# Optimization experiments

Measured on AMD Instinct MI355X. Metric: run time of the kernel, lower is better.

Reference implementation:

```python
import jax, jax.numpy as jnp
import numpy as np

H = 2048  # hidden_dim == input_dim


def _lstm_step(x, h, c, Wih, Whh, bih, bhh):
    # x: [1, in], h/c: [1, H]; PyTorch gate order: i, f, g, o along 4H axis
    gates = x @ Wih.T + h @ Whh.T + bih + bhh  # [1, 4H]
    i, f, g, o = jnp.split(gates, 4, axis=-1)
    c2 = jax.nn.sigmoid(f) * c + jax.nn.sigmoid(i) * jnp.tanh(g)
    h2 = jax.nn.sigmoid(o) * jnp.tanh(c2)
    return h2, c2


def setup_inputs() -> dict:
    key = jax.random.key(0)
    ks = jax.random.split(key, 20)
    s = 0.02
    inp = {
        "x": jax.random.normal(ks[0], (1,), dtype=jnp.float32),
        "input_hidden": jax.random.normal(ks[1], (3, 1, H), dtype=jnp.float32),
        "input_cell": jax.random.normal(ks[2], (3, 1, H), dtype=jnp.float32),
        # layer 0: input_size = 1
        "Wih0": jax.random.normal(ks[3], (4 * H, 1), dtype=jnp.float32) * s,
        "Whh0": jax.random.normal(ks[4], (4 * H, H), dtype=jnp.float32) * s,
        "bih0": jax.random.normal(ks[5], (4 * H,), dtype=jnp.float32) * s,
        "bhh0": jax.random.normal(ks[6], (4 * H,), dtype=jnp.float32) * s,
        # layers 1, 2: input_size = H
        "Wih1": jax.random.normal(ks[7], (4 * H, H), dtype=jnp.float32) * s,
        "Whh1": jax.random.normal(ks[8], (4 * H, H), dtype=jnp.float32) * s,
        "bih1": jax.random.normal(ks[9], (4 * H,), dtype=jnp.float32) * s,
        "bhh1": jax.random.normal(ks[10], (4 * H,), dtype=jnp.float32) * s,
        "Wih2": jax.random.normal(ks[11], (4 * H, H), dtype=jnp.float32) * s,
        "Whh2": jax.random.normal(ks[12], (4 * H, H), dtype=jnp.float32) * s,
        "bih2": jax.random.normal(ks[13], (4 * H,), dtype=jnp.float32) * s,
        "bhh2": jax.random.normal(ks[14], (4 * H,), dtype=jnp.float32) * s,
        # output projection: Linear(H, 1)
        "Wout": jax.random.normal(ks[15], (1, H), dtype=jnp.float32) * s,
        "bout": jax.random.normal(ks[16], (1,), dtype=jnp.float32) * s,
    }
    return inp


def reference(x, input_hidden, input_cell,
              Wih0, Whh0, bih0, bhh0,
              Wih1, Whh1, bih1, bhh1,
              Wih2, Whh2, bih2, bhh2,
              Wout, bout):
    # x.reshape((1,1,1)) in torch -> single timestep, batch 1, feature 1
    inp = x.reshape(1, 1)  # [batch=1, in=1]
    params = [(Wih0, Whh0, bih0, bhh0),
              (Wih1, Whh1, bih1, bhh1),
              (Wih2, Whh2, bih2, bhh2)]
    hs, cs = [], []
    layer_in = inp
    for l, (Wih, Whh, bih, bhh) in enumerate(params):  # fixed 3 layers
        h2, c2 = _lstm_step(layer_in, input_hidden[l], input_cell[l], Wih, Whh, bih, bhh)
        hs.append(h2)
        cs.append(c2)
        layer_in = h2
    hidden_n = jnp.stack(hs, axis=0)  # [3, 1, H]
    cell_n = jnp.stack(cs, axis=0)    # [3, 1, H]
    # top-layer output [1,1,H] -> Linear -> [1,1,1]
    y = (layer_in @ Wout.T + bout).reshape(1, 1, 1)
    return y, hidden_n, cell_n
```

## Files before the change

### kernel.cpp

```cpp
#include <hip/hip_runtime.h>
#include <math.h>

#define H 2048

__device__ __forceinline__ float sigmoidf_(float v) {
    return 1.0f / (1.0f + expf(-v));
}

__device__ __forceinline__ float wave_reduce_sum(float v) {
    v += __shfl_down(v, 32, 64);
    v += __shfl_down(v, 16, 64);
    v += __shfl_down(v, 8, 64);
    v += __shfl_down(v, 4, 64);
    v += __shfl_down(v, 2, 64);
    v += __shfl_down(v, 1, 64);
    return v;
}

__global__ __launch_bounds__(256)
void lstm_layer0(const float* __restrict__ Wih0,
                 const float* __restrict__ Whh,
                 const float* __restrict__ bih,
                 const float* __restrict__ bhh,
                 const float* __restrict__ xs,
                 const float* __restrict__ hin,
                 const float* __restrict__ cin,
                 float* __restrict__ hout,
                 float* __restrict__ cout)
{
    __shared__ float hv[H];
    __shared__ float dots[4];
    const int t = blockIdx.x;
    const int tid = threadIdx.x;

    {
        const float4* h4 = (const float4*)hin;
        float4* hs = (float4*)hv;
        hs[tid] = h4[tid];
        hs[tid + 256] = h4[tid + 256];
    }
    __syncthreads();

    const int w = tid >> 6;
    const int lane = tid & 63;
    const size_t row = (size_t)w * H + t;
    const float4* Wr = (const float4*)(Whh + row * H);
    const float4* v4 = (const float4*)hv;

    float acc = 0.0f;
#pragma unroll
    for (int k = 0; k < 8; ++k) {
        float4 a = Wr[lane + 64 * k];
        float4 b = v4[lane + 64 * k];
        acc += a.x * b.x + a.y * b.y + a.z * b.z + a.w * b.w;
    }
    acc = wave_reduce_sum(acc);
    if (lane == 0) dots[w] = acc;
    __syncthreads();

    if (tid == 0) {
        const float x = xs[0];
        float gi = dots[0] + x * Wih0[t]         + bih[t]         + bhh[t];
        float gf = dots[1] + x * Wih0[H + t]     + bih[H + t]     + bhh[H + t];
        float gg = dots[2] + x * Wih0[2 * H + t] + bih[2 * H + t] + bhh[2 * H + t];
        float go = dots[3] + x * Wih0[3 * H + t] + bih[3 * H + t] + bhh[3 * H + t];
        float c2 = sigmoidf_(gf) * cin[t] + sigmoidf_(gi) * tanhf(gg);
        float h2 = sigmoidf_(go) * tanhf(c2);
        cout[t] = c2;
        hout[t] = h2;
    }
}

__global__ __launch_bounds__(512)
void lstm_layer_mat(const float* __restrict__ Wih,
                    const float* __restrict__ Whh,
                    const float* __restrict__ bih,
                    const float* __restrict__ bhh,
                    const float* __restrict__ xin,
                    const float* __restrict__ hin,
                    const float* __restrict__ cin,
                    float* __restrict__ hout,
                    float* __restrict__ cout)
{
    __shared__ float xv[H];
    __shared__ float hv[H];
    __shared__ float dots[8];
    const int t = blockIdx.x;
    const int tid = threadIdx.x;

    {
        const float4* x4 = (const float4*)xin;
        const float4* h4 = (const float4*)hin;
        ((float4*)xv)[tid] = x4[tid];
        ((float4*)hv)[tid] = h4[tid];
    }
    __syncthreads();

    const int w = tid >> 6;
    const int lane = tid & 63;
    const int gate = w & 3;
    const float* W = (w < 4) ? Wih : Whh;
    const float* v = (w < 4) ? xv : hv;
    const size_t row = (size_t)gate * H + t;
    const float4* Wr = (const float4*)(W + row * H);
    const float4* v4 = (const float4*)v;

    float acc = 0.0f;
#pragma unroll
    for (int k = 0; k < 8; ++k) {
        float4 a = Wr[lane + 64 * k];
        float4 b = v4[lane + 64 * k];
        acc += a.x * b.x + a.y * b.y + a.z * b.z + a.w * b.w;
    }
    acc = wave_reduce_sum(acc);
    if (lane == 0) dots[w] = acc;
    __syncthreads();

    if (tid == 0) {
        float gi = dots[0] + dots[4] + bih[t]         + bhh[t];
        float gf = dots[1] + dots[5] + bih[H + t]     + bhh[H + t];
        float gg = dots[2] + dots[6] + bih[2 * H + t] + bhh[2 * H + t];
        float go = dots[3] + dots[7] + bih[3 * H + t] + bhh[3 * H + t];
        float c2 = sigmoidf_(gf) * cin[t] + sigmoidf_(gi) * tanhf(gg);
        float h2 = sigmoidf_(go) * tanhf(c2);
        cout[t] = c2;
        hout[t] = h2;
    }
}

__global__ __launch_bounds__(256)
void out_proj(const float* __restrict__ Wout,
              const float* __restrict__ bout,
              const float* __restrict__ h,
              float* __restrict__ y)
{
    __shared__ float part[4];
    const int tid = threadIdx.x;
    const float4* W4 = (const float4*)Wout;
    const float4* h4 = (const float4*)h;
    float acc = 0.0f;
#pragma unroll
    for (int k = 0; k < 2; ++k) {
        int i = tid + 256 * k;
        float4 a = W4[i];
        float4 b = h4[i];
        acc += a.x * b.x + a.y * b.y + a.z * b.z + a.w * b.w;
    }
    acc = wave_reduce_sum(acc);
    if ((tid & 63) == 0) part[tid >> 6] = acc;
    __syncthreads();
    if (tid == 0) y[0] = part[0] + part[1] + part[2] + part[3] + bout[0];
}

extern "C" void kernel_launch(void* const* d_in, const int* in_sizes, int n_in,
                              void* d_out, int out_size, void* d_ws, size_t ws_size,
                              hipStream_t stream) {
    const float* x    = (const float*)d_in[0];
    const float* hin  = (const float*)d_in[1];
    const float* cin  = (const float*)d_in[2];
    const float* Wih0 = (const float*)d_in[3];
    const float* Whh0 = (const float*)d_in[4];
    const float* bih0 = (const float*)d_in[5];
    const float* bhh0 = (const float*)d_in[6];
    const float* Wih1 = (const float*)d_in[7];
    const float* Whh1 = (const float*)d_in[8];
    const float* bih1 = (const float*)d_in[9];
    const float* bhh1 = (const float*)d_in[10];
    const float* Wih2 = (const float*)d_in[11];
    const float* Whh2 = (const float*)d_in[12];
    const float* bih2 = (const float*)d_in[13];
    const float* bhh2 = (const float*)d_in[14];
    const float* Wout = (const float*)d_in[15];
    const float* bout = (const float*)d_in[16];

    float* out = (float*)d_out;
    float* y  = out;
    float* hN = out + 1;
    float* cN = out + 1 + 3 * H;

    lstm_layer0<<<H, 256, 0, stream>>>(Wih0, Whh0, bih0, bhh0, x,
                                       hin, cin, hN, cN);
    lstm_layer_mat<<<H, 512, 0, stream>>>(Wih1, Whh1, bih1, bhh1,
                                          hN, hin + H, cin + H,
                                          hN + H, cN + H);
    lstm_layer_mat<<<H, 512, 0, stream>>>(Wih2, Whh2, bih2, bhh2,
                                          hN + H, hin + 2 * H, cin + 2 * H,
                                          hN + 2 * H, cN + 2 * H);
    out_proj<<<1, 256, 0, stream>>>(Wout, bout, hN + 2 * H, y);
}
```

Before: 323.8 us.

## Split LSTM layers into partial-dot and combine kernels with direct global-to-LDS loads

Each layer's gate matvec is split into a partial kernel, with one block per (matrix, hidden unit) writing biased dot products to workspace. A small elementwise combine kernel then applies the gate nonlinearities. Weight rows are streamed with global_load_lds straight into LDS, and the input vectors are held in registers instead of being staged in shared memory. The aim is more, smaller blocks and better memory-level parallelism for the bandwidth-bound weight reads, at the cost of three extra kernel launches and a workspace round-trip.

```diff
diff --git a/kernel.cpp b/kernel.cpp
--- a/kernel.cpp
+++ b/kernel.cpp
@@ -17,115 +17,125 @@
     return v;
 }
 
-__global__ __launch_bounds__(256)
-void lstm_layer0(const float* __restrict__ Wih0,
-                 const float* __restrict__ Whh,
-                 const float* __restrict__ bih,
-                 const float* __restrict__ bhh,
-                 const float* __restrict__ xs,
-                 const float* __restrict__ hin,
-                 const float* __restrict__ cin,
-                 float* __restrict__ hout,
-                 float* __restrict__ cout)
-{
-    __shared__ float hv[H];
-    __shared__ float dots[4];
-    const int t = blockIdx.x;
-    const int tid = threadIdx.x;
-
-    {
-        const float4* h4 = (const float4*)hin;
-        float4* hs = (float4*)hv;
-        hs[tid] = h4[tid];
-        hs[tid + 256] = h4[tid + 256];
-    }
+__device__ __forceinline__ void gl_lds16(const float* gsrc, float* lds_dst) {
+    __builtin_amdgcn_global_load_lds(
+        (const __attribute__((address_space(1))) void*)gsrc,
+        (__attribute__((address_space(3))) void*)lds_dst,
+        16, 0, 0);
+}
+
+__global__ __launch_bounds__(256)
+void lstm_partial(const float* __restrict__ Wih, const float* __restrict__ Whh,
+                  const float* __restrict__ bih, const float* __restrict__ bhh,
+                  const float* __restrict__ xin,
+                  const float* __restrict__ hin,
+                  float* __restrict__ part)
+{
+    __shared__ float4 wbuf[4][512];
+    const int bid = blockIdx.x;
+    const int m = bid >> 11;
+    const int t = bid & 2047;
+    const int w = threadIdx.x >> 6;
+    const int lane = threadIdx.x & 63;
+
+    const float* W = m ? Whh : Wih;
+    const float* v = m ? hin : xin;
+    const float* barr = m ? bhh : bih;
+    const float* row = W + (size_t)(w * H + t) * H;
+    float* lbase = (float*)&wbuf[w][0];
+
+#pragma unroll
+    for (int k = 0; k < 8; ++k)
+        gl_lds16(row + k * 256 + lane * 4, lbase + k * 256);
+
+    float4 bv[8];
+    const float4* v4 = (const float4*)v;
+#pragma unroll
+    for (int k = 0; k < 8; ++k) bv[k] = v4[lane + 64 * k];
+    const float bias = barr[w * H + t];
+
     __syncthreads();
 
-    const int w = tid >> 6;
-    const int lane = tid & 63;
-    const size_t row = (size_t)w * H + t;
-    const float4* Wr = (const float4*)(Whh + row * H);
-    const float4* v4 = (const float4*)hv;
-
     float acc = 0.0f;
+    const float4* lb4 = &wbuf[w][0];
 #pragma unroll
     for (int k = 0; k < 8; ++k) {
-        float4 a = Wr[lane + 64 * k];
-        float4 b = v4[lane + 64 * k];
-        acc += a.x * b.x + a.y * b.y + a.z * b.z + a.w * b.w;
+        float4 a = lb4[k * 64 + lane];
+        acc += a.x * bv[k].x + a.y * bv[k].y + a.z * bv[k].z + a.w * bv[k].w;
     }
     acc = wave_reduce_sum(acc);
-    if (lane == 0) dots[w] = acc;
+    if (lane == 0) part[m * 4 * H + w * H + t] = acc + bias;
+}
+
+__global__ __launch_bounds__(256)
+void lstm0_partial(const float* __restrict__ Whh,
+                   const float* __restrict__ bih, const float* __restrict__ bhh,
+                   const float* __restrict__ hin,
+                   float* __restrict__ part)
+{
+    __shared__ float4 wbuf[4][512];
+    const int t = blockIdx.x;
+    const int w = threadIdx.x >> 6;
+    const int lane = threadIdx.x & 63;
+
+    const float* row = Whh + (size_t)(w * H + t) * H;
+    float* lbase = (float*)&wbuf[w][0];
+#pragma unroll
+    for (int k = 0; k < 8; ++k)
+        gl_lds16(row + k * 256 + lane * 4, lbase + k * 256);
+
+    float4 bv[8];
+    const float4* v4 = (const float4*)hin;
+#pragma unroll
+    for (int k = 0; k < 8; ++k) bv[k] = v4[lane + 64 * k];
+    const float bias = bih[w * H + t] + bhh[w * H + t];
+
     __syncthreads();
 
-    if (tid == 0) {
-        const float x = xs[0];
-        float gi = dots[0] + x * Wih0[t]         + bih[t]         + bhh[t];
-        float gf = dots[1] + x * Wih0[H + t]     + bih[H + t]     + bhh[H + t];
-        float gg = dots[2] + x * Wih0[2 * H + t] + bih[2 * H + t] + bhh[2 * H + t];
-        float go = dots[3] + x * Wih0[3 * H + t] + bih[3 * H + t] + bhh[3 * H + t];
-        float c2 = sigmoidf_(gf) * cin[t] + sigmoidf_(gi) * tanhf(gg);
-        float h2 = sigmoidf_(go) * tanhf(c2);
-        cout[t] = c2;
-        hout[t] = h2;
-    }
-}
-
-__global__ __launch_bounds__(512)
-void lstm_layer_mat(const float* __restrict__ Wih,
-                    const float* __restrict__ Whh,
-                    const float* __restrict__ bih,
-                    const float* __restrict__ bhh,
-                    const float* __restrict__ xin,
-                    const float* __restrict__ hin,
-                    const float* __restrict__ cin,
-                    float* __restrict__ hout,
-                    float* __restrict__ cout)
-{
-    __shared__ float xv[H];
-    __shared__ float hv[H];
-    __shared__ float dots[8];
-    const int t = blockIdx.x;
-    const int tid = threadIdx.x;
-
-    {
-        const float4* x4 = (const float4*)xin;
-        const float4* h4 = (const float4*)hin;
-        ((float4*)xv)[tid] = x4[tid];
-        ((float4*)hv)[tid] = h4[tid];
-    }
-    __syncthreads();
-
-    const int w = tid >> 6;
-    const int lane = tid & 63;
-    const int gate = w & 3;
-    const float* W = (w < 4) ? Wih : Whh;
-    const float* v = (w < 4) ? xv : hv;
-    const size_t row = (size_t)gate * H + t;
-    const float4* Wr = (const float4*)(W + row * H);
-    const float4* v4 = (const float4*)v;
-
     float acc = 0.0f;
+    const float4* lb4 = &wbuf[w][0];
 #pragma unroll
     for (int k = 0; k < 8; ++k) {
-        float4 a = Wr[lane + 64 * k];
-        float4 b = v4[lane + 64 * k];
-        acc += a.x * b.x + a.y * b.y + a.z * b.z + a.w * b.w;
+        float4 a = lb4[k * 64 + lane];
+        acc += a.x * bv[k].x + a.y * bv[k].y + a.z * bv[k].z + a.w * bv[k].w;
     }
     acc = wave_reduce_sum(acc);
-    if (lane == 0) dots[w] = acc;
-    __syncthreads();
-
-    if (tid == 0) {
-        float gi = dots[0] + dots[4] + bih[t]         + bhh[t];
-        float gf = dots[1] + dots[5] + bih[H + t]     + bhh[H + t];
-        float gg = dots[2] + dots[6] + bih[2 * H + t] + bhh[2 * H + t];
-        float go = dots[3] + dots[7] + bih[3 * H + t] + bhh[3 * H + t];
-        float c2 = sigmoidf_(gf) * cin[t] + sigmoidf_(gi) * tanhf(gg);
-        float h2 = sigmoidf_(go) * tanhf(c2);
-        cout[t] = c2;
-        hout[t] = h2;
-    }
+    if (lane == 0) part[w * H + t] = acc + bias;
+}
+
+__global__ __launch_bounds__(256)
+void lstm_combine(const float* __restrict__ part,
+                  const float* __restrict__ cin,
+                  float* __restrict__ hout, float* __restrict__ cout)
+{
+    const int t = blockIdx.x * 256 + threadIdx.x;
+    float gi = part[t]         + part[4 * H + t];
+    float gf = part[H + t]     + part[5 * H + t];
+    float gg = part[2 * H + t] + part[6 * H + t];
+    float go = part[3 * H + t] + part[7 * H + t];
+    float c2 = sigmoidf_(gf) * cin[t] + sigmoidf_(gi) * tanhf(gg);
+    float h2 = sigmoidf_(go) * tanhf(c2);
+    cout[t] = c2;
+    hout[t] = h2;
+}
+
+__global__ __launch_bounds__(256)
+void lstm0_combine(const float* __restrict__ part,
+                   const float* __restrict__ Wih0,
+                   const float* __restrict__ xs,
+                   const float* __restrict__ cin,
+                   float* __restrict__ hout, float* __restrict__ cout)
+{
+    const int t = blockIdx.x * 256 + threadIdx.x;
+    const float x = xs[0];
+    float gi = part[t]         + x * Wih0[t];
+    float gf = part[H + t]     + x * Wih0[H + t];
+    float gg = part[2 * H + t] + x * Wih0[2 * H + t];
+    float go = part[3 * H + t] + x * Wih0[3 * H + t];
+    float c2 = sigmoidf_(gf) * cin[t] + sigmoidf_(gi) * tanhf(gg);
+    float h2 = sigmoidf_(go) * tanhf(c2);
+    cout[t] = c2;
+    hout[t] = h2;
 }
 
 __global__ __launch_bounds__(256)
@@ -134,7 +144,7 @@
               const float* __restrict__ h,
               float* __restrict__ y)
 {
-    __shared__ float part[4];
+    __shared__ float partl[4];
     const int tid = threadIdx.x;
     const float4* W4 = (const float4*)Wout;
     const float4* h4 = (const float4*)h;
@@ -147,9 +157,9 @@
         acc += a.x * b.x + a.y * b.y + a.z * b.z + a.w * b.w;
     }
     acc = wave_reduce_sum(acc);
-    if ((tid & 63) == 0) part[tid >> 6] = acc;
+    if ((tid & 63) == 0) partl[tid >> 6] = acc;
     __syncthreads();
-    if (tid == 0) y[0] = part[0] + part[1] + part[2] + part[3] + bout[0];
+    if (tid == 0) y[0] = partl[0] + partl[1] + partl[2] + partl[3] + bout[0];
 }
 
 extern "C" void kernel_launch(void* const* d_in, const int* in_sizes, int n_in,
@@ -178,13 +188,18 @@
     float* hN = out + 1;
     float* cN = out + 1 + 3 * H;
 
-    lstm_layer0<<<H, 256, 0, stream>>>(Wih0, Whh0, bih0, bhh0, x,
-                                       hin, cin, hN, cN);
-    lstm_layer_mat<<<H, 512, 0, stream>>>(Wih1, Whh1, bih1, bhh1,
-                                          hN, hin + H, cin + H,
-                                          hN + H, cN + H);
-    lstm_layer_mat<<<H, 512, 0, stream>>>(Wih2, Whh2, bih2, bhh2,
-                                          hN + H, hin + 2 * H, cin + 2 * H,
-                                          hN + 2 * H, cN + 2 * H);
+    float* part = (float*)d_ws;
+
+    lstm0_partial<<<2048, 256, 0, stream>>>(Whh0, bih0, bhh0, hin, part);
+    lstm0_combine<<<8, 256, 0, stream>>>(part, Wih0, x, cin, hN, cN);
+
+    lstm_partial<<<4096, 256, 0, stream>>>(Wih1, Whh1, bih1, bhh1,
+                                           hN, hin + H, part);
+    lstm_combine<<<8, 256, 0, stream>>>(part, cin + H, hN + H, cN + H);
+
+    lstm_partial<<<4096, 256, 0, stream>>>(Wih2, Whh2, bih2, bhh2,
+                                           hN + H, hin + 2 * H, part);
+    lstm_combine<<<8, 256, 0, stream>>>(part, cin + 2 * H, hN + 2 * H, cN + 2 * H);
+
     out_proj<<<1, 256, 0, stream>>>(Wout, bout, hN + 2 * H, y);
 }
```

Result: slower. 335.9 us (+3.7%).
